# Kernel optimization log

Hardware: AMD Instinct MI355X
Metric: run time of the kernel (lower is better)

The kernel has to match this reference:

```python
import jax, jax.numpy as jnp
import numpy as np

LQ, LK, B, E, H = 1024, 1024, 8, 1024, 16


def setup_inputs() -> dict:
    key0 = jax.random.key(0)
    ks = jax.random.split(key0, 6)
    std = float(np.sqrt(2.0 / (E + E)))
    query = jax.random.normal(ks[0], (LQ, B, E), dtype=jnp.float32)
    key = jax.random.normal(ks[1], (LK, B, E), dtype=jnp.float32)
    attn_mask = jax.random.randint(ks[2], (B, LK), 0, 2).astype(bool)
    in_proj_weight_q = std * jax.random.normal(ks[3], (E, E), dtype=jnp.float32)
    in_proj_weight_kv = std * jax.random.normal(ks[4], (2 * E, E), dtype=jnp.float32)
    out_proj_weight = std * jax.random.normal(ks[5], (E, E), dtype=jnp.float32)
    return {
        "query": query,
        "key": key,
        "attn_mask": attn_mask,
        "in_proj_weight_q": in_proj_weight_q,
        "in_proj_weight_kv": in_proj_weight_kv,
        "out_proj_weight": out_proj_weight,
        "num_heads": H,
    }


def reference(query, key, attn_mask, in_proj_weight_q, in_proj_weight_kv, out_proj_weight, num_heads):
    Lq, Bs, Em = query.shape
    Lk = key.shape[0]
    Hd = Em // num_heads  # head_dim
    scaling = Hd ** (-0.5)

    # input projections: F.linear(x, W) == x @ W.T  (no bias)
    q = jnp.einsum("lbe,fe->lbf", query, in_proj_weight_q) * scaling
    kv = jnp.einsum("lbe,fe->lbf", key, in_proj_weight_kv)
    k, v = jnp.split(kv, 2, axis=-1)

    # [len, b, e] -> [b, h, len, d]
    def to_heads(x, L):
        return x.reshape(L, Bs, num_heads, Hd).transpose(1, 2, 0, 3)

    qh = to_heads(q, Lq)
    kh = to_heads(k, Lk)
    vh = to_heads(v, Lk)

    scores = jnp.einsum("bhqd,bhkd->bhqk", qh, kh)  # [B,H,Lq,Lk]
    neg = jnp.asarray(-1e9, scores.dtype)
    scores = jnp.where(attn_mask[:, None, None, :], neg, scores)
    attn = jax.nn.softmax(scores, axis=-1)  # coverage (dropout=0, eval)

    ctx = jnp.einsum("bhqk,bhkd->bhqd", attn, vh)  # [B,H,Lq,d]
    ctx = ctx.transpose(2, 0, 1, 3).reshape(Lq, Bs, Em)
    out = jnp.einsum("lbe,fe->lbf", ctx, out_proj_weight)
    return out, attn
```

## Files before the change

kernel.cpp:

```cpp
#include <hip/hip_runtime.h>
#include <hip/hip_bf16.h>
#include <cstdint>
#include <cstddef>

constexpr int LQc = 1024, LKc = 1024, Bc = 8, Ec = 1024, Hc = 16, Dc = 64;

typedef __bf16 bf16;
typedef __bf16 bf16x4 __attribute__((ext_vector_type(4)));
typedef __bf16 bf16x8 __attribute__((ext_vector_type(8)));
typedef float  f32x4  __attribute__((ext_vector_type(4)));

#define MFMA16(a, b, c) __builtin_amdgcn_mfma_f32_16x16x32_bf16((a), (b), (c), 0, 0, 0)

__device__ __forceinline__ void gload_lds16(const bf16* g, bf16* l) {
  __builtin_amdgcn_global_load_lds((const __attribute__((address_space(1))) void*)g,
                                   (__attribute__((address_space(3))) void*)l, 16, 0, 0);
}

__global__ __launch_bounds__(256) void k_convert(const float* __restrict__ q,
                                                 const float* __restrict__ k,
                                                 const float* __restrict__ wq,
                                                 const float* __restrict__ wkv,
                                                 const float* __restrict__ wout,
                                                 bf16* __restrict__ dst) {
  const size_t i = ((size_t)blockIdx.x * 256 + threadIdx.x) * 8;
  const float* src; size_t off; float sc = 1.0f;
  if (i < 8388608)        { src = q;    off = i; sc = 0.125f; }
  else if (i < 16777216)  { src = k;    off = i - 8388608; }
  else if (i < 17825792)  { src = wq;   off = i - 16777216; }
  else if (i < 19922944)  { src = wkv;  off = i - 17825792; }
  else                    { src = wout; off = i - 19922944; }
  const f32x4 a = *reinterpret_cast<const f32x4*>(src + off);
  const f32x4 b = *reinterpret_cast<const f32x4*>(src + off + 4);
  bf16x8 o;
  o[0] = (bf16)(a.x * sc); o[1] = (bf16)(a.y * sc);
  o[2] = (bf16)(a.z * sc); o[3] = (bf16)(a.w * sc);
  o[4] = (bf16)(b.x * sc); o[5] = (bf16)(b.y * sc);
  o[6] = (bf16)(b.z * sc); o[7] = (bf16)(b.w * sc);
  *reinterpret_cast<bf16x8*>(dst + i) = o;
}

template <int MODE>
__global__ __launch_bounds__(256) void k_gemm(const bf16* __restrict__ Aq,
                                              const bf16* __restrict__ Ak,
                                              const bf16* __restrict__ Wq,
                                              const bf16* __restrict__ Wkv,
                                              bf16* __restrict__ q3,
                                              bf16* __restrict__ k3,
                                              bf16* __restrict__ v3,
                                              float* __restrict__ o_f) {
  __shared__ bf16 As[128 * 32];
  __shared__ bf16 Bs[128 * 32];

  const int tid  = threadIdx.x;
  const int lane = tid & 63, wave = tid >> 6;
  const int wm = wave & 1, wn = wave >> 1;

  const int cpx = gridDim.x >> 3;
  const int logical = (blockIdx.x & 7) * cpx + (blockIdx.x >> 3);
  const int bx = logical & 63, by = logical >> 6;
  const int m0 = bx * 128;

  const bf16* Ap;
  const bf16* Wp;
  bf16* Op = nullptr;
  if constexpr (MODE == 0) {
    if (by < 8)       { Ap = Aq; Wp = Wq  + (size_t)by * 131072;        Op = q3; }
    else if (by < 16) { Ap = Ak; Wp = Wkv + (size_t)(by - 8) * 131072;  Op = k3; }
    else              { Ap = Ak; Wp = Wkv + 1048576 + (size_t)(by - 16) * 131072; Op = v3; }
  } else {
    Ap = Aq; Wp = Wq + (size_t)by * 131072;
  }
  const int col0 = (by & 7) * 128;

  const int fr = lane & 15, fo = (lane >> 4) * 8;

  f32x4 acc[4][4] = {};

  const int srow = lane >> 2;
  const int scol = (lane & 3) * 8;
  const bf16* ga = Ap + (size_t)(m0 + wave * 32 + srow) * Ec + scol;
  const bf16* gb = Wp + (size_t)(wave * 32 + srow) * Ec + scol;
  bf16* lA = As + wave * 1024;
  bf16* lB = Bs + wave * 1024;

  for (int k0 = 0; k0 < Ec; k0 += 32) {
    gload_lds16(ga + k0, lA);
    gload_lds16(ga + k0 + 16 * Ec, lA + 512);
    gload_lds16(gb + k0, lB);
    gload_lds16(gb + k0 + 16 * Ec, lB + 512);
    __syncthreads();

    bf16x8 a[4], b[4];
#pragma unroll
    for (int i = 0; i < 4; ++i) {
      a[i] = *reinterpret_cast<const bf16x8*>(As + (wm * 64 + i * 16 + fr) * 32 + fo);
      b[i] = *reinterpret_cast<const bf16x8*>(Bs + (wn * 64 + i * 16 + fr) * 32 + fo);
    }
#pragma unroll
    for (int i = 0; i < 4; ++i)
#pragma unroll
      for (int j = 0; j < 4; ++j) acc[i][j] = MFMA16(a[i], b[j], acc[i][j]);
    __syncthreads();
  }

  const int rb = (lane >> 4) * 4;
#pragma unroll
  for (int i = 0; i < 4; ++i) {
#pragma unroll
    for (int j = 0; j < 4; ++j) {
      const int col = col0 + wn * 64 + j * 16 + fr;
#pragma unroll
      for (int r = 0; r < 4; ++r) {
        const int tok = m0 + wm * 64 + i * 16 + rb + r;
        const float val = acc[i][j][r];
        if constexpr (MODE == 0) {
          Op[(size_t)tok * Ec + col] = (bf16)val;
        } else {
          o_f[(size_t)tok * Ec + col] = val;
        }
      }
    }
  }
}

__global__ __launch_bounds__(256) void k_vtrans(const bf16* __restrict__ v3,
                                                bf16* __restrict__ VhT) {
  __shared__ bf16 tile[64][72];
  const int bh = blockIdx.y;
  const int b = bh >> 4, h = bh & 15;
  const int l0 = blockIdx.x * 64;
  const int r = threadIdx.x >> 3, c = (threadIdx.x & 7) * 8;
#pragma unroll
  for (int rr = 0; rr < 2; ++rr) {
    const int lk = rr * 32 + r;
    *reinterpret_cast<bf16x8*>(&tile[lk][c]) =
        *reinterpret_cast<const bf16x8*>(v3 + ((size_t)(l0 + lk) * Bc + b) * Ec + h * Dc + c);
  }
  __syncthreads();
#pragma unroll
  for (int rr = 0; rr < 2; ++rr) {
    const int d = rr * 32 + r;
    bf16x8 o;
#pragma unroll
    for (int j = 0; j < 8; ++j) o[j] = tile[c + j][d];
    *reinterpret_cast<bf16x8*>(VhT + ((size_t)bh * Dc + d) * LKc + l0 + c) = o;
  }
}

__global__ __launch_bounds__(256) void k_attn(const bf16* __restrict__ q3,
                                              const bf16* __restrict__ k3,
                                              const bf16* __restrict__ VhT,
                                              const int* __restrict__ mask,
                                              float* __restrict__ attn_out,
                                              bf16* __restrict__ ctx_out) {
  __shared__ bf16 sP[32][1032];
  __shared__ float smask[1024];
  __shared__ float psum[4][32];
  __shared__ float rinv[32];

  const int tid = threadIdx.x;
  const int lane = tid & 63, wave = tid >> 6;

  int flat = blockIdx.x;
  flat = (flat & 7) * 512 + (flat >> 3);
  const int bh = flat >> 5;
  const int q0 = (flat & 31) * 32;
  const int b = bh >> 4, h = bh & 15;
  const int fr = lane & 15, fo = (lane >> 4) * 8, rb = (lane >> 4) * 4;

  for (int c = tid; c < 1024; c += 256)
    smask[c] = mask[b * LKc + c] ? -1e9f : 0.0f;

  bf16x8 qf[2][2];
  const bf16* Qb = q3 + ((size_t)q0 * Bc + b) * Ec + h * Dc;
#pragma unroll
  for (int m = 0; m < 2; ++m)
#pragma unroll
    for (int kc = 0; kc < 2; ++kc)
      qf[m][kc] = *reinterpret_cast<const bf16x8*>(
          Qb + (size_t)(m * 16 + fr) * (Bc * Ec) + kc * 32 + fo);
  __syncthreads();

  const bf16* Kb = k3 + (size_t)b * Ec + h * Dc;
  float s0[4] = {0.f, 0.f, 0.f, 0.f}, s1[4] = {0.f, 0.f, 0.f, 0.f};
  for (int t = 0; t < 16; ++t) {
    const int n = (wave * 16 + t) * 16;
    const bf16* kp = Kb + (size_t)(n + fr) * (Bc * Ec) + fo;
    const bf16x8 kf0 = *reinterpret_cast<const bf16x8*>(kp);
    const bf16x8 kf1 = *reinterpret_cast<const bf16x8*>(kp + 32);
    f32x4 c0 = {}, c1 = {};
    c0 = MFMA16(qf[0][0], kf0, c0);
    c0 = MFMA16(qf[0][1], kf1, c0);
    c1 = MFMA16(qf[1][0], kf0, c1);
    c1 = MFMA16(qf[1][1], kf1, c1);
    const int col = n + fr;
    const float madd = smask[col];
#pragma unroll
    for (int r = 0; r < 4; ++r) {
      const float e0 = __expf(c0[r] + madd);
      const float e1 = __expf(c1[r] + madd);
      s0[r] += e0; s1[r] += e1;
      sP[rb + r][col]      = (bf16)e0;
      sP[16 + rb + r][col] = (bf16)e1;
    }
  }
#pragma unroll
  for (int o = 1; o < 16; o <<= 1)
#pragma unroll
    for (int r = 0; r < 4; ++r) {
      s0[r] += __shfl_xor(s0[r], o, 64);
      s1[r] += __shfl_xor(s1[r], o, 64);
    }
  if (fr == 0) {
#pragma unroll
    for (int r = 0; r < 4; ++r) {
      psum[wave][rb + r]      = s0[r];
      psum[wave][16 + rb + r] = s1[r];
    }
  }
  __syncthreads();
  if (tid < 32)
    rinv[tid] = 1.0f / (psum[0][tid] + psum[1][tid] + psum[2][tid] + psum[3][tid]);
  __syncthreads();

  float* ap = attn_out + ((size_t)bh * LQc + q0) * LKc;
  for (int r = 0; r < 32; ++r) {
    const float rs = rinv[r];
    const bf16x4 v = *reinterpret_cast<const bf16x4*>(&sP[r][tid * 4]);
    f32x4 p;
    p.x = (float)v.x * rs; p.y = (float)v.y * rs;
    p.z = (float)v.z * rs; p.w = (float)v.w * rs;
    *reinterpret_cast<f32x4*>(ap + (size_t)r * LKc + tid * 4) = p;
  }

  const bf16* Vb = VhT + ((size_t)bh * Dc + wave * 16 + fr) * LKc;
  f32x4 cacc0 = {}, cacc1 = {};
  for (int kc = 0; kc < 1024; kc += 32) {
    const bf16x8 vf  = *reinterpret_cast<const bf16x8*>(Vb + kc + fo);
    const bf16x8 pa0 = *reinterpret_cast<const bf16x8*>(&sP[fr][kc + fo]);
    const bf16x8 pa1 = *reinterpret_cast<const bf16x8*>(&sP[16 + fr][kc + fo]);
    cacc0 = MFMA16(pa0, vf, cacc0);
    cacc1 = MFMA16(pa1, vf, cacc1);
  }
  const int e = h * Dc + wave * 16 + fr;
#pragma unroll
  for (int r = 0; r < 4; ++r) {
    const int qa = q0 + rb + r;
    ctx_out[((size_t)qa * Bc + b) * Ec + e] = (bf16)(cacc0[r] * rinv[rb + r]);
    const int qb2 = q0 + 16 + rb + r;
    ctx_out[((size_t)qb2 * Bc + b) * Ec + e] = (bf16)(cacc1[r] * rinv[16 + rb + r]);
  }
}

extern "C" void kernel_launch(void* const* d_in, const int* in_sizes, int n_in,
                              void* d_out, int out_size, void* d_ws, size_t ws_size,
                              hipStream_t stream) {
  const float* query = (const float*)d_in[0];
  const float* keyx  = (const float*)d_in[1];
  const int*   mask  = (const int*)d_in[2];
  const float* wq    = (const float*)d_in[3];
  const float* wkv   = (const float*)d_in[4];
  const float* wout  = (const float*)d_in[5];

  float* out  = (float*)d_out;
  float* attn = out + (size_t)LQc * Bc * Ec;

  bf16* cvt   = (bf16*)d_ws;
  bf16* q2    = cvt;
  bf16* k2    = q2   + 8388608;
  bf16* wqb   = k2   + 8388608;
  bf16* wkvb  = wqb  + 1048576;
  bf16* woutb = wkvb + 2097152;
  bf16* q3    = woutb + 1048576;
  bf16* k3    = q3   + 8388608;
  bf16* v3    = k3   + 8388608;
  bf16* vt    = q2;
  bf16* ctx   = k2;

  k_convert<<<10240, 256, 0, stream>>>(query, keyx, wq, wkv, wout, cvt);
  k_gemm<0><<<1536, 256, 0, stream>>>(q2, k2, wqb, wkvb, q3, k3, v3, nullptr);
  k_vtrans<<<dim3(16, 128), 256, 0, stream>>>(v3, vt);
  k_attn<<<4096, 256, 0, stream>>>(q3, k3, vt, mask, attn, ctx);
  k_gemm<2><<<512, 256, 0, stream>>>(ctx, nullptr, woutb, nullptr, nullptr, nullptr, nullptr, out);
}
```

Baseline: 359.8 us.

## Store projections in head-major layout and overlap attn writes with PV MFMA

The QKV projection epilogue now writes Q, K, V in [b,h,len,d] head-major layout, so the attention and V-transpose kernels read contiguous 64-element rows instead of strided rows 16 KB apart. The attention kernel interleaves the fp32 attention-probability stores with the PV MFMA loop rather than running them as separate phases, so global writes can overlap with matrix math. It also raises wave priority around MFMA groups with s_setprio. The GEMM epilogue's scattered bf16 stores become less coalesced across tokens, which may cost some write efficiency.

```diff
diff --git a/kernel.cpp b/kernel.cpp
--- a/kernel.cpp
+++ b/kernel.cpp
@@ -45,9 +45,9 @@
                                               const bf16* __restrict__ Ak,
                                               const bf16* __restrict__ Wq,
                                               const bf16* __restrict__ Wkv,
-                                              bf16* __restrict__ q3,
-                                              bf16* __restrict__ k3,
-                                              bf16* __restrict__ v3,
+                                              bf16* __restrict__ qh,
+                                              bf16* __restrict__ kh,
+                                              bf16* __restrict__ vh,
                                               float* __restrict__ o_f) {
   __shared__ bf16 As[128 * 32];
   __shared__ bf16 Bs[128 * 32];
@@ -65,9 +65,9 @@
   const bf16* Wp;
   bf16* Op = nullptr;
   if constexpr (MODE == 0) {
-    if (by < 8)       { Ap = Aq; Wp = Wq  + (size_t)by * 131072;        Op = q3; }
-    else if (by < 16) { Ap = Ak; Wp = Wkv + (size_t)(by - 8) * 131072;  Op = k3; }
-    else              { Ap = Ak; Wp = Wkv + 1048576 + (size_t)(by - 16) * 131072; Op = v3; }
+    if (by < 8)       { Ap = Aq; Wp = Wq  + (size_t)by * 131072;        Op = qh; }
+    else if (by < 16) { Ap = Ak; Wp = Wkv + (size_t)(by - 8) * 131072;  Op = kh; }
+    else              { Ap = Ak; Wp = Wkv + 1048576 + (size_t)(by - 16) * 131072; Op = vh; }
   } else {
     Ap = Aq; Wp = Wq + (size_t)by * 131072;
   }
@@ -115,7 +115,9 @@
         const int tok = m0 + wm * 64 + i * 16 + rb + r;
         const float val = acc[i][j][r];
         if constexpr (MODE == 0) {
-          Op[(size_t)tok * Ec + col] = (bf16)val;
+          const int lq = tok >> 3, bb = tok & 7;
+          const int h = col >> 6, dd = col & 63;
+          Op[(((size_t)(bb * Hc + h)) * LQc + lq) * Dc + dd] = (bf16)val;
         } else {
           o_f[(size_t)tok * Ec + col] = val;
         }
@@ -124,18 +126,17 @@
   }
 }
 
-__global__ __launch_bounds__(256) void k_vtrans(const bf16* __restrict__ v3,
+__global__ __launch_bounds__(256) void k_vtrans(const bf16* __restrict__ Vh,
                                                 bf16* __restrict__ VhT) {
   __shared__ bf16 tile[64][72];
   const int bh = blockIdx.y;
-  const int b = bh >> 4, h = bh & 15;
   const int l0 = blockIdx.x * 64;
   const int r = threadIdx.x >> 3, c = (threadIdx.x & 7) * 8;
 #pragma unroll
   for (int rr = 0; rr < 2; ++rr) {
-    const int lk = rr * 32 + r;
-    *reinterpret_cast<bf16x8*>(&tile[lk][c]) =
-        *reinterpret_cast<const bf16x8*>(v3 + ((size_t)(l0 + lk) * Bc + b) * Ec + h * Dc + c);
+    const int row = rr * 32 + r;
+    *reinterpret_cast<bf16x8*>(&tile[row][c]) =
+        *reinterpret_cast<const bf16x8*>(Vh + ((size_t)bh * LKc + l0 + row) * Dc + c);
   }
   __syncthreads();
 #pragma unroll
@@ -148,8 +149,8 @@
   }
 }
 
-__global__ __launch_bounds__(256) void k_attn(const bf16* __restrict__ q3,
-                                              const bf16* __restrict__ k3,
+__global__ __launch_bounds__(256) void k_attn(const bf16* __restrict__ Qh,
+                                              const bf16* __restrict__ Kh,
                                               const bf16* __restrict__ VhT,
                                               const int* __restrict__ mask,
                                               float* __restrict__ attn_out,
@@ -173,27 +174,28 @@
     smask[c] = mask[b * LKc + c] ? -1e9f : 0.0f;
 
   bf16x8 qf[2][2];
-  const bf16* Qb = q3 + ((size_t)q0 * Bc + b) * Ec + h * Dc;
+  const bf16* Qb = Qh + ((size_t)bh * LQc + q0) * Dc;
 #pragma unroll
   for (int m = 0; m < 2; ++m)
 #pragma unroll
     for (int kc = 0; kc < 2; ++kc)
-      qf[m][kc] = *reinterpret_cast<const bf16x8*>(
-          Qb + (size_t)(m * 16 + fr) * (Bc * Ec) + kc * 32 + fo);
-  __syncthreads();
-
-  const bf16* Kb = k3 + (size_t)b * Ec + h * Dc;
+      qf[m][kc] = *reinterpret_cast<const bf16x8*>(Qb + (size_t)(m * 16 + fr) * Dc + kc * 32 + fo);
+  __syncthreads();
+
+  const bf16* Kb = Kh + (size_t)bh * LKc * Dc;
   float s0[4] = {0.f, 0.f, 0.f, 0.f}, s1[4] = {0.f, 0.f, 0.f, 0.f};
   for (int t = 0; t < 16; ++t) {
     const int n = (wave * 16 + t) * 16;
-    const bf16* kp = Kb + (size_t)(n + fr) * (Bc * Ec) + fo;
+    const bf16* kp = Kb + (size_t)(n + fr) * Dc + fo;
     const bf16x8 kf0 = *reinterpret_cast<const bf16x8*>(kp);
     const bf16x8 kf1 = *reinterpret_cast<const bf16x8*>(kp + 32);
     f32x4 c0 = {}, c1 = {};
+    __builtin_amdgcn_s_setprio(1);
     c0 = MFMA16(qf[0][0], kf0, c0);
     c0 = MFMA16(qf[0][1], kf1, c0);
     c1 = MFMA16(qf[1][0], kf0, c1);
     c1 = MFMA16(qf[1][1], kf1, c1);
+    __builtin_amdgcn_s_setprio(0);
     const int col = n + fr;
     const float madd = smask[col];
 #pragma unroll
@@ -225,24 +227,25 @@
   __syncthreads();
 
   float* ap = attn_out + ((size_t)bh * LQc + q0) * LKc;
-  for (int r = 0; r < 32; ++r) {
-    const float rs = rinv[r];
-    const bf16x4 v = *reinterpret_cast<const bf16x4*>(&sP[r][tid * 4]);
+  const bf16* Vb = VhT + ((size_t)bh * Dc + wave * 16 + fr) * LKc;
+  f32x4 cacc0 = {}, cacc1 = {};
+  for (int s = 0; s < 32; ++s) {
+    const int kc = s * 32;
+    const bf16x8 vf  = *reinterpret_cast<const bf16x8*>(Vb + kc + fo);
+    const bf16x8 pa0 = *reinterpret_cast<const bf16x8*>(&sP[fr][kc + fo]);
+    const bf16x8 pa1 = *reinterpret_cast<const bf16x8*>(&sP[16 + fr][kc + fo]);
+    __builtin_amdgcn_s_setprio(1);
+    cacc0 = MFMA16(pa0, vf, cacc0);
+    cacc1 = MFMA16(pa1, vf, cacc1);
+    __builtin_amdgcn_s_setprio(0);
+    const float rs = rinv[s];
+    const bf16x4 v = *reinterpret_cast<const bf16x4*>(&sP[s][tid * 4]);
     f32x4 p;
     p.x = (float)v.x * rs; p.y = (float)v.y * rs;
     p.z = (float)v.z * rs; p.w = (float)v.w * rs;
-    *reinterpret_cast<f32x4*>(ap + (size_t)r * LKc + tid * 4) = p;
-  }
-
-  const bf16* Vb = VhT + ((size_t)bh * Dc + wave * 16 + fr) * LKc;
-  f32x4 cacc0 = {}, cacc1 = {};
-  for (int kc = 0; kc < 1024; kc += 32) {
-    const bf16x8 vf  = *reinterpret_cast<const bf16x8*>(Vb + kc + fo);
-    const bf16x8 pa0 = *reinterpret_cast<const bf16x8*>(&sP[fr][kc + fo]);
-    const bf16x8 pa1 = *reinterpret_cast<const bf16x8*>(&sP[16 + fr][kc + fo]);
-    cacc0 = MFMA16(pa0, vf, cacc0);
-    cacc1 = MFMA16(pa1, vf, cacc1);
-  }
+    *reinterpret_cast<f32x4*>(ap + (size_t)s * LKc + tid * 4) = p;
+  }
+
   const int e = h * Dc + wave * 16 + fr;
 #pragma unroll
   for (int r = 0; r < 4; ++r) {
@@ -272,15 +275,15 @@
   bf16* wqb   = k2   + 8388608;
   bf16* wkvb  = wqb  + 1048576;
   bf16* woutb = wkvb + 2097152;
-  bf16* q3    = woutb + 1048576;
-  bf16* k3    = q3   + 8388608;
-  bf16* v3    = k3   + 8388608;
+  bf16* qh    = woutb + 1048576;
+  bf16* kh    = qh   + 8388608;
+  bf16* vh    = kh   + 8388608;
   bf16* vt    = q2;
   bf16* ctx   = k2;
 
   k_convert<<<10240, 256, 0, stream>>>(query, keyx, wq, wkv, wout, cvt);
-  k_gemm<0><<<1536, 256, 0, stream>>>(q2, k2, wqb, wkvb, q3, k3, v3, nullptr);
-  k_vtrans<<<dim3(16, 128), 256, 0, stream>>>(v3, vt);
-  k_attn<<<4096, 256, 0, stream>>>(q3, k3, vt, mask, attn, ctx);
+  k_gemm<0><<<1536, 256, 0, stream>>>(q2, k2, wqb, wkvb, qh, kh, vh, nullptr);
+  k_vtrans<<<dim3(16, 128), 256, 0, stream>>>(vh, vt);
+  k_attn<<<4096, 256, 0, stream>>>(qh, kh, vt, mask, attn, ctx);
   k_gemm<2><<<512, 256, 0, stream>>>(ctx, nullptr, woutb, nullptr, nullptr, nullptr, nullptr, out);
 }
```

New measurement: 412.9 us. +14.8%, slower.
